# Optimization experiments

Hardware: AMD Instinct MI355X
Metric: run time of the kernel (lower is better)

## Reference

```python
import jax, jax.numpy as jnp
import numpy as np

D = 512           # embedding_dim
K = 4096          # num_embeddings
COMMITMENT_COST = 0.25


def setup_inputs() -> dict:
    key = jax.random.key(0)
    k1, k2 = jax.random.split(key)
    x = jax.random.normal(k1, (32, 32, 32, D), dtype=jnp.float32)
    # glorot-normal-ish init for the [D, K] codebook
    emb = jax.random.normal(k2, (D, K), dtype=jnp.float32) * np.float32(np.sqrt(2.0 / (D + K)))
    return {"x": x, "embeddings": emb}


def reference(x, embeddings):
    # x: [B, H, W, D]; embeddings: [D, K]
    flat = x.reshape(-1, D)  # [N, D]
    n = flat.shape[0]
    distances = (jnp.sum(flat * flat, axis=1, keepdims=True)
                 - 2.0 * (flat @ embeddings)
                 + jnp.sum(embeddings * embeddings, axis=0, keepdims=True))
    encoding_indices = jnp.argmin(distances, axis=1)  # [N]
    quantized = jnp.take(embeddings.T, encoding_indices, axis=0).reshape(x.shape)

    e_latent_loss = jnp.mean((jax.lax.stop_gradient(quantized) - x) ** 2)
    q_latent_loss = jnp.mean((quantized - jax.lax.stop_gradient(x)) ** 2)
    loss = q_latent_loss + COMMITMENT_COST * e_latent_loss

    # straight-through estimator
    quantized_st = x + jax.lax.stop_gradient(quantized - x)

    # perplexity without materializing the [N, K] one-hot
    avg_probs = jnp.zeros((K,), dtype=x.dtype).at[encoding_indices].add(1.0) / n
    perplexity = jnp.exp(-jnp.sum(avg_probs * jnp.log(avg_probs + 1e-10)))

    return quantized_st, loss, perplexity
```

## Files before the change

### kernel.cpp

```cpp
#include <hip/hip_runtime.h>
#include <stdint.h>

#define DD 512
#define KK 4096
#define NN 32768

typedef __attribute__((ext_vector_type(8))) short bf16x8;
typedef __attribute__((ext_vector_type(4))) float f32x4;

__device__ __forceinline__ unsigned short bf16_rn(float f) {
  uint32_t u = __float_as_uint(f);
  return (unsigned short)((u + 0x7FFFu + ((u >> 16) & 1u)) >> 16);
}

__global__ __launch_bounds__(256) void conv_x_kernel(const float4* __restrict__ x4,
                                                     unsigned short* __restrict__ xh) {
  int gid = blockIdx.x * 256 + threadIdx.x;
  float4 a = x4[gid * 2];
  float4 b = x4[gid * 2 + 1];
  union { unsigned short u[8]; uint4 q; } H;
  H.u[0] = bf16_rn(a.x); H.u[1] = bf16_rn(a.y);
  H.u[2] = bf16_rn(a.z); H.u[3] = bf16_rn(a.w);
  H.u[4] = bf16_rn(b.x); H.u[5] = bf16_rn(b.y);
  H.u[6] = bf16_rn(b.z); H.u[7] = bf16_rn(b.w);
  *(uint4*)(xh + (size_t)gid * 8) = H.q;
}

template <bool WRITE_ET>
__global__ __launch_bounds__(256) void prep_et_kernel(const float* __restrict__ E,
                                                      unsigned short* __restrict__ Eth,
                                                      float* __restrict__ he2,
                                                      float* __restrict__ Et) {
  __shared__ float t[32][33];
  int bk = (blockIdx.x & 127) * 32;
  int bd = (blockIdx.x >> 7) * 32;
  int c = threadIdx.x & 31;
  int r0 = threadIdx.x >> 5;
#pragma unroll
  for (int r = r0; r < 32; r += 8) t[r][c] = E[(size_t)(bd + r) * KK + bk + c];
  __syncthreads();
#pragma unroll
  for (int i = 0; i < 4; ++i) {
    int r = r0 + i * 8;
    float v = t[c][r];
    size_t o = (size_t)(bk + r) * DD + bd + c;
    Eth[o] = bf16_rn(v);
    if (WRITE_ET) Et[o] = v;
    float v2 = v * v;
#pragma unroll
    for (int m = 1; m < 32; m <<= 1) v2 += __shfl_xor(v2, m, 64);
    if (c == 0) atomicAdd(&he2[bk + r], 0.5f * v2);
  }
}

#define ANB 512
#define BN 128

__device__ __forceinline__ void stage_tile(const unsigned short* __restrict__ xh,
                                           const unsigned short* __restrict__ Eth,
                                           char* Ah, char* Bh, int block_m, int ncode,
                                           int dt, int w, int srow, int schunk) {
#pragma unroll
  for (int r = 0; r < 4; ++r) {
    const int rowbase = w * 32 + r * 8;
    const int arow = block_m + rowbase + srow;
    const int brow = ncode + rowbase + srow;
    const int col = dt + schunk * 8;
    __builtin_amdgcn_global_load_lds(
        (const __attribute__((address_space(1))) void*)(xh + (size_t)arow * DD + col),
        (__attribute__((address_space(3))) void*)(Ah + rowbase * 128), 16, 0, 0);
    __builtin_amdgcn_global_load_lds(
        (const __attribute__((address_space(1))) void*)(Eth + (size_t)brow * DD + col),
        (__attribute__((address_space(3))) void*)(Bh + rowbase * 128), 16, 0, 0);
  }
}

__global__ __launch_bounds__(256, 2) void argmax_mfma_kernel(
    const unsigned short* __restrict__ xh, const unsigned short* __restrict__ Eth,
    const float* __restrict__ he2, unsigned long long* __restrict__ best64) {
  __shared__ __align__(16) char smem[65536];

  const int tid = threadIdx.x;
  const int w = tid >> 6;
  const int lane = tid & 63;
  const int wm = w >> 1, wk = w & 1;
  const int l15 = lane & 15, quad = lane >> 4;

  const int orig = blockIdx.x;
  const int wgid = (orig & 7) * 256 + (orig >> 3);
  const int block_m = (wgid >> 3) * BN;
  const int nbase = (wgid & 7) * ANB;

  const int srow = lane >> 3;
  const int schunk = (lane & 7) ^ (lane >> 3);
  const int rx = l15 & 7;

  float best[16];
  int bidx[16];
#pragma unroll
  for (int s = 0; s < 16; ++s) { best[s] = -INFINITY; bidx[s] = 0; }

  stage_tile(xh, Eth, smem, smem + 16384, block_m, nbase, 0, w, srow, schunk);
  __syncthreads();
  int cur = 0;

  for (int nt = 0; nt < 4; ++nt) {
    const int ncode = nbase + nt * BN;
    f32x4 acc[4][4];
#pragma unroll
    for (int ti = 0; ti < 4; ++ti)
#pragma unroll
      for (int tj = 0; tj < 4; ++tj) acc[ti][tj] = (f32x4){0.f, 0.f, 0.f, 0.f};

    for (int dtI = 0; dtI < 8; ++dtI) {
      char* nAh = smem + (cur ^ 1) * 32768;
      if (dtI < 7) {
        stage_tile(xh, Eth, nAh, nAh + 16384, block_m, ncode, (dtI + 1) * 64, w, srow,
                   schunk);
      } else if (nt < 3) {
        stage_tile(xh, Eth, nAh, nAh + 16384, block_m, ncode + BN, 0, w, srow, schunk);
      }

      char* Ah = smem + cur * 32768;
      char* Bh = Ah + 16384;
#pragma unroll
      for (int s = 0; s < 2; ++s) {
        const int ch = ((s * 4 + quad) ^ rx) * 16;
        bf16x8 af[4], bfv[4];
#pragma unroll
        for (int t = 0; t < 4; ++t) {
          af[t] = *(const bf16x8*)(Ah + (wm * 64 + t * 16 + l15) * 128 + ch);
          bfv[t] = *(const bf16x8*)(Bh + (wk * 64 + t * 16 + l15) * 128 + ch);
        }
#pragma unroll
        for (int ti = 0; ti < 4; ++ti)
#pragma unroll
          for (int tj = 0; tj < 4; ++tj)
            acc[ti][tj] = __builtin_amdgcn_mfma_f32_16x16x32_bf16(af[ti], bfv[tj],
                                                                  acc[ti][tj], 0, 0, 0);
      }
      __syncthreads();
      cur ^= 1;
    }

    const int colb = ncode + wk * 64 + l15;
#pragma unroll
    for (int tj = 0; tj < 4; ++tj) {
      float h = he2[colb + tj * 16];
#pragma unroll
      for (int ti = 0; ti < 4; ++ti)
#pragma unroll
        for (int r = 0; r < 4; ++r) {
          float sc = acc[ti][tj][r] - h;
          int slot = ti * 4 + r;
          if (sc > best[slot]) { best[slot] = sc; bidx[slot] = colb + tj * 16; }
        }
    }
  }

#pragma unroll
  for (int slot = 0; slot < 16; ++slot) {
    float v = best[slot];
    int ii = bidx[slot];
#pragma unroll
    for (int m = 1; m < 16; m <<= 1) {
      float ov = __shfl_xor(v, m, 64);
      int oi = __shfl_xor(ii, m, 64);
      if (ov > v || (ov == v && oi < ii)) { v = ov; ii = oi; }
    }
    if (l15 == 0) {
      int row = block_m + wm * 64 + (slot >> 2) * 16 + quad * 4 + (slot & 3);
      uint32_t b = __float_as_uint(v);
      uint32_t mm = (b & 0x80000000u) ? ~b : (b | 0x80000000u);
      unsigned long long packed = ((unsigned long long)mm << 32) | (uint32_t)(~(uint32_t)ii);
      atomicMax(&best64[row], packed);
    }
  }
}

#define BM 128
#define BK 128
#define KS 4
#define KPB (KK / KS)
#define BD 32

__global__ __launch_bounds__(256, 4) void argmax_kernel(
    const float* __restrict__ x, const float* __restrict__ E,
    const float* __restrict__ he2, unsigned long long* __restrict__ best64) {
  __shared__ __align__(16) char smem[33280];
  float (*xs)[132] = (float (*)[132])smem;
  float (*es)[BK] = (float (*)[BK])(smem + 16896);

  const int tid = threadIdx.x;
  const int wave = tid >> 6;
  const int lane = tid & 63;
  const int wm = wave >> 1, wk = wave & 1;
  const int tm = lane >> 3, tk = lane & 7;
  const int block_m = (blockIdx.x >> 2) * BM;
  const int kbase = (blockIdx.x & 3) * KPB;

  float best[8];
  int bidx[8];
#pragma unroll
  for (int i = 0; i < 8; ++i) { best[i] = -INFINITY; bidx[i] = 0; }

  const int xtok = tid >> 3;
  const int xd4 = tid & 7;
  const int erow_lane = (lane >> 5);
  const int ecol = (lane & 31) * 4;

  for (int kt = 0; kt < KPB; kt += BK) {
    const int k0 = kbase + kt;
    float acc[8][8];
#pragma unroll
    for (int i = 0; i < 8; ++i)
#pragma unroll
      for (int j = 0; j < 8; ++j) acc[i][j] = 0.f;

    for (int dt = 0; dt < DD; dt += BD) {
      __syncthreads();
#pragma unroll
      for (int r = 0; r < 4; ++r) {
        int row = r * 8 + wave * 2;
        const float* gp = E + (size_t)(dt + row + erow_lane) * KK + k0 + ecol;
        __builtin_amdgcn_global_load_lds(
            (const __attribute__((address_space(1))) void*)gp,
            (__attribute__((address_space(3))) void*)&es[row][0], 16, 0, 0);
      }
#pragma unroll
      for (int r = 0; r < 4; ++r) {
        int tok = xtok + r * 32;
        float4 v = *(const float4*)(x + (size_t)(block_m + tok) * DD + dt + xd4 * 4);
        xs[xd4 * 4 + 0][tok] = v.x;
        xs[xd4 * 4 + 1][tok] = v.y;
        xs[xd4 * 4 + 2][tok] = v.z;
        xs[xd4 * 4 + 3][tok] = v.w;
      }
      __syncthreads();
#pragma unroll 4
      for (int d = 0; d < BD; ++d) {
        const float4 a0 = *(const float4*)&xs[d][wm * 64 + tm * 8];
        const float4 a1 = *(const float4*)&xs[d][wm * 64 + tm * 8 + 4];
        const float4 b0 = *(const float4*)&es[d][wk * 64 + tk * 8];
        const float4 b1 = *(const float4*)&es[d][wk * 64 + tk * 8 + 4];
        const float av[8] = {a0.x, a0.y, a0.z, a0.w, a1.x, a1.y, a1.z, a1.w};
        const float bv[8] = {b0.x, b0.y, b0.z, b0.w, b1.x, b1.y, b1.z, b1.w};
#pragma unroll
        for (int i = 0; i < 8; ++i)
#pragma unroll
          for (int j = 0; j < 8; ++j) acc[i][j] = fmaf(av[i], bv[j], acc[i][j]);
      }
    }
    const int kcol = k0 + wk * 64 + tk * 8;
    float4 h0 = *(const float4*)(he2 + kcol);
    float4 h1 = *(const float4*)(he2 + kcol + 4);
    const float hv[8] = {h0.x, h0.y, h0.z, h0.w, h1.x, h1.y, h1.z, h1.w};
#pragma unroll
    for (int i = 0; i < 8; ++i) {
#pragma unroll
      for (int j = 0; j < 8; ++j) {
        float s = acc[i][j] - hv[j];
        if (s > best[i]) { best[i] = s; bidx[i] = kcol + j; }
      }
    }
  }

  __syncthreads();
  float (*rv)[17] = (float (*)[17])smem;
  int (*ri)[17] = (int (*)[17])(smem + 8704);
#pragma unroll
  for (int i = 0; i < 8; ++i) {
    int tok = wm * 64 + tm * 8 + i;
    rv[tok][wk * 8 + tk] = best[i];
    ri[tok][wk * 8 + tk] = bidx[i];
  }
  __syncthreads();
  if (tid < BM) {
    float bv = rv[tid][0];
    int bi = ri[tid][0];
#pragma unroll
    for (int t = 1; t < 16; ++t) {
      float v = rv[tid][t];
      int ii = ri[tid][t];
      if (v > bv || (v == bv && ii < bi)) { bv = v; bi = ii; }
    }
    uint32_t b = __float_as_uint(bv);
    uint32_t m = (b & 0x80000000u) ? ~b : (b | 0x80000000u);
    unsigned long long packed = ((unsigned long long)m << 32) | (uint32_t)(~(uint32_t)bi);
    atomicMax(&best64[block_m + tid], packed);
  }
}

__global__ __launch_bounds__(256) void gather_et_kernel(
    const float* __restrict__ x, const float* __restrict__ Et,
    const unsigned long long* __restrict__ best64, float* __restrict__ out,
    float* __restrict__ partials, int* __restrict__ counts) {
  __shared__ float sh[256];
  int tid = threadIdx.x;
  int gid = blockIdx.x * 256 + tid;
  int n = gid >> 7;
  int d4 = gid & 127;
  int k = (int)(~(uint32_t)best64[n]);
  float4 q = *(const float4*)(Et + (size_t)k * DD + d4 * 4);
  float4 xv = *(const float4*)(x + (size_t)n * DD + d4 * 4);
  *(float4*)(out + (size_t)n * DD + d4 * 4) = q;
  float dx0 = q.x - xv.x, dx1 = q.y - xv.y, dx2 = q.z - xv.z, dx3 = q.w - xv.w;
  sh[tid] = dx0 * dx0 + dx1 * dx1 + dx2 * dx2 + dx3 * dx3;
  if (d4 == 0) atomicAdd(&counts[k], 1);
  __syncthreads();
  for (int s = 128; s > 0; s >>= 1) {
    if (tid < s) sh[tid] += sh[tid + s];
    __syncthreads();
  }
  if (tid == 0) atomicAdd(&partials[blockIdx.x & 255], sh[0]);
}

__global__ __launch_bounds__(256) void gather_direct_kernel(
    const float* __restrict__ x, const float* __restrict__ E,
    const unsigned long long* __restrict__ best64, float* __restrict__ out,
    float* __restrict__ partials, int* __restrict__ counts) {
  __shared__ float sh[256];
  int tid = threadIdx.x;
  int gid = blockIdx.x * 256 + tid;
  int n = gid >> 7;
  int d4 = gid & 127;
  int k = (int)(~(uint32_t)best64[n]);
  float4 q;
  q.x = E[(size_t)(d4 * 4 + 0) * KK + k];
  q.y = E[(size_t)(d4 * 4 + 1) * KK + k];
  q.z = E[(size_t)(d4 * 4 + 2) * KK + k];
  q.w = E[(size_t)(d4 * 4 + 3) * KK + k];
  float4 xv = *(const float4*)(x + (size_t)n * DD + d4 * 4);
  *(float4*)(out + (size_t)n * DD + d4 * 4) = q;
  float dx0 = q.x - xv.x, dx1 = q.y - xv.y, dx2 = q.z - xv.z, dx3 = q.w - xv.w;
  sh[tid] = dx0 * dx0 + dx1 * dx1 + dx2 * dx2 + dx3 * dx3;
  if (d4 == 0) atomicAdd(&counts[k], 1);
  __syncthreads();
  for (int s = 128; s > 0; s >>= 1) {
    if (tid < s) sh[tid] += sh[tid + s];
    __syncthreads();
  }
  if (tid == 0) atomicAdd(&partials[blockIdx.x & 255], sh[0]);
}

__global__ __launch_bounds__(256) void finalize_kernel(
    const int* __restrict__ counts, const float* __restrict__ partials,
    float* __restrict__ out) {
  __shared__ float sh[256];
  int tid = threadIdx.x;
  float h = 0.f;
  for (int k = tid; k < KK; k += 256) {
    float p = (float)counts[k] * (1.0f / (float)NN);
    h += p * logf(p + 1e-10f);
  }
  sh[tid] = h;
  __syncthreads();
  for (int s = 128; s > 0; s >>= 1) {
    if (tid < s) sh[tid] += sh[tid + s];
    __syncthreads();
  }
  float H = sh[0];
  __syncthreads();
  sh[tid] = partials[tid];
  __syncthreads();
  for (int s = 128; s > 0; s >>= 1) {
    if (tid < s) sh[tid] += sh[tid + s];
    __syncthreads();
  }
  if (tid == 0) {
    float mse = sh[0] / (float)((size_t)NN * DD);
    out[(size_t)NN * DD] = 1.25f * mse;
    out[(size_t)NN * DD + 1] = expf(-H);
  }
}

extern "C" void kernel_launch(void* const* d_in, const int* in_sizes, int n_in,
                              void* d_out, int out_size, void* d_ws, size_t ws_size,
                              hipStream_t stream) {
  const float* x = (const float*)d_in[0];
  const float* E = (const float*)d_in[1];
  float* out = (float*)d_out;
  char* ws = (char*)d_ws;

  unsigned long long* best64 = (unsigned long long*)(ws + 0);
  float* he2 = (float*)(ws + 262144);
  int* counts = (int*)(ws + 278528);
  float* partials = (float*)(ws + 294912);
  unsigned short* Eth = (unsigned short*)(ws + 295936);
  float* Et = (float*)(ws + 4490240);
  const size_t NEED_MFMA = 4490240;
  const size_t NEED_ET = 4490240 + (size_t)DD * KK * 4;

  hipMemsetAsync(ws, 0, 295936, stream);

  if (ws_size >= NEED_MFMA) {
    unsigned short* xh = (unsigned short*)d_out;
    const bool use_et = ws_size >= NEED_ET;

    conv_x_kernel<<<(NN * DD / 8) / 256, 256, 0, stream>>>((const float4*)x, xh);
    if (use_et)
      prep_et_kernel<true><<<(KK / 32) * (DD / 32), 256, 0, stream>>>(E, Eth, he2, Et);
    else
      prep_et_kernel<false><<<(KK / 32) * (DD / 32), 256, 0, stream>>>(E, Eth, he2, Et);
    argmax_mfma_kernel<<<(NN / 128) * 8, 256, 0, stream>>>(xh, Eth, he2, best64);
    if (use_et)
      gather_et_kernel<<<(NN * (DD / 4)) / 256, 256, 0, stream>>>(x, Et, best64, out,
                                                                  partials, counts);
    else
      gather_direct_kernel<<<(NN * (DD / 4)) / 256, 256, 0, stream>>>(x, E, best64, out,
                                                                      partials, counts);
  } else {
    prep_et_kernel<false><<<(KK / 32) * (DD / 32), 256, 0, stream>>>(
        E, (unsigned short*)(ws + 295936), he2, (float*)nullptr);
    argmax_kernel<<<(NN / BM) * KS, 256, 0, stream>>>(x, E, he2, best64);
    gather_direct_kernel<<<(NN * (DD / 4)) / 256, 256, 0, stream>>>(x, E, best64, out,
                                                                    partials, counts);
  }
  finalize_kernel<<<1, 256, 0, stream>>>(counts, partials, out);
}
```

Measured before the change: 320.4 us.

## Replace full syncthreads with partial vmcnt waits and raw barriers in GEMM pipeline

Swaps the __syncthreads calls in the double-buffered distance GEMM for explicit s_waitcnt vmcnt(8) waits plus raw s_barrier. This lets the next tile's global loads stay in flight while the current tile is consumed, rather than draining all memory ops at each barrier. It also preloads the codebook norm values into registers before the main loop and unrolls the outer tile loop. Correctness now depends on stage_tile issuing exactly 8 loads per thread in the assumed order, and on whether the LDS writes are tracked by these waits; any mismatch would race.

New measurement: 414.3 us. 1.29x slower.

```diff
diff --git a/kernel.cpp b/kernel.cpp
--- a/kernel.cpp
+++ b/kernel.cpp
@@ -95,15 +95,21 @@
   const int schunk = (lane & 7) ^ (lane >> 3);
   const int rx = l15 & 7;
 
+  float hv[16];
+#pragma unroll
+  for (int nt = 0; nt < 4; ++nt)
+#pragma unroll
+    for (int tj = 0; tj < 4; ++tj)
+      hv[nt * 4 + tj] = he2[nbase + nt * BN + wk * 64 + l15 + tj * 16];
+
   float best[16];
   int bidx[16];
 #pragma unroll
   for (int s = 0; s < 16; ++s) { best[s] = -INFINITY; bidx[s] = 0; }
 
   stage_tile(xh, Eth, smem, smem + 16384, block_m, nbase, 0, w, srow, schunk);
-  __syncthreads();
-  int cur = 0;
-
+
+#pragma unroll
   for (int nt = 0; nt < 4; ++nt) {
     const int ncode = nbase + nt * BN;
     f32x4 acc[4][4];
@@ -113,16 +119,25 @@
       for (int tj = 0; tj < 4; ++tj) acc[ti][tj] = (f32x4){0.f, 0.f, 0.f, 0.f};
 
     for (int dtI = 0; dtI < 8; ++dtI) {
-      char* nAh = smem + (cur ^ 1) * 32768;
+      char* curbuf = smem + (size_t)((dtI & 1) * 32768);
+      char* nxtbuf = smem + (size_t)(((dtI + 1) & 1) * 32768);
+
       if (dtI < 7) {
-        stage_tile(xh, Eth, nAh, nAh + 16384, block_m, ncode, (dtI + 1) * 64, w, srow,
+        stage_tile(xh, Eth, nxtbuf, nxtbuf + 16384, block_m, ncode, (dtI + 1) * 64, w,
+                   srow, schunk);
+        asm volatile("s_waitcnt vmcnt(8)" ::: "memory");
+      } else if (nt < 3) {
+        stage_tile(xh, Eth, nxtbuf, nxtbuf + 16384, block_m, ncode + BN, 0, w, srow,
                    schunk);
-      } else if (nt < 3) {
-        stage_tile(xh, Eth, nAh, nAh + 16384, block_m, ncode + BN, 0, w, srow, schunk);
-      }
-
-      char* Ah = smem + cur * 32768;
-      char* Bh = Ah + 16384;
+        asm volatile("s_waitcnt vmcnt(8)" ::: "memory");
+      } else {
+        asm volatile("s_waitcnt vmcnt(0)" ::: "memory");
+      }
+      __builtin_amdgcn_s_barrier();
+      asm volatile("" ::: "memory");
+
+      char* Ah = curbuf;
+      char* Bh = curbuf + 16384;
 #pragma unroll
       for (int s = 0; s < 2; ++s) {
         const int ch = ((s * 4 + quad) ^ rx) * 16;
@@ -139,14 +154,14 @@
             acc[ti][tj] = __builtin_amdgcn_mfma_f32_16x16x32_bf16(af[ti], bfv[tj],
                                                                   acc[ti][tj], 0, 0, 0);
       }
-      __syncthreads();
-      cur ^= 1;
+      asm volatile("" ::: "memory");
+      __builtin_amdgcn_s_barrier();
     }
 
     const int colb = ncode + wk * 64 + l15;
 #pragma unroll
     for (int tj = 0; tj < 4; ++tj) {
-      float h = he2[colb + tj * 16];
+      float h = hv[nt * 4 + tj];
 #pragma unroll
       for (int ti = 0; ti < 4; ++ti)
 #pragma unroll
```
